# Kernel optimization log

Measured on AMD Instinct MI355X. Metric: run time of the kernel, lower is better.

The kernel has to match this reference:

```python
import jax, jax.numpy as jnp
import numpy as np

D_MODEL = 512; D_STATE = 128; D_CONV = 4; EXPAND = 2; HEADDIM = 64; CHUNK = 64
D_INNER = EXPAND * D_MODEL            # 1024
NHEADS = D_INNER // HEADDIM           # 16
CONV_DIM = D_INNER + 2 * D_STATE      # 1280
D_IN_PROJ = 2 * D_INNER + 2 * D_STATE + NHEADS  # 2320
BATCH, SEQLEN = 2, 8192


def setup_inputs() -> dict:
    key = jax.random.key(0)
    ks = jax.random.split(key, 8)
    s = 0.02
    return {
        "x": jax.random.normal(ks[0], (BATCH, SEQLEN, D_MODEL), jnp.float32),
        "in_proj_w": jax.random.normal(ks[1], (D_IN_PROJ, D_MODEL), jnp.float32) * s,
        "conv_w": jax.random.normal(ks[2], (CONV_DIM, 1, D_CONV), jnp.float32) * s,
        "conv_b": jnp.zeros((CONV_DIM,), jnp.float32),
        "dt_bias": jax.random.normal(ks[3], (NHEADS,), jnp.float32) * s,
        "A_log": jnp.log(jnp.arange(1, NHEADS + 1, dtype=jnp.float32)),
        "D_skip": jnp.ones((NHEADS,), jnp.float32),
        "norm_w": jnp.ones((D_INNER,), jnp.float32),
        "ssm_out_w": jax.random.normal(ks[4], (D_MODEL, D_INNER), jnp.float32) * s,
        "fuse_w": jax.random.normal(ks[5], (D_MODEL, 2 * D_MODEL), jnp.float32) * s,
        "fuse_b": jnp.zeros((D_MODEL,), jnp.float32),
    }


def segsum(a):
    # a: (..., T) -> (..., T, T) with [i, j] = sum_{j < d <= i} a[d]; -inf above diag
    T = a.shape[-1]
    a = jnp.broadcast_to(a[..., :, None], a.shape + (T,))
    a = jnp.where(jnp.tril(jnp.ones((T, T), bool), -1), a, 0.0)
    a = jnp.cumsum(a, axis=-2)
    return jnp.where(jnp.tril(jnp.ones((T, T), bool), 0), a, -jnp.inf)


def ssd(x, A, B, C):
    # x: (b,l,h,p), A: (b,l,h), B/C: (b,l,n) (single group, broadcast over heads)
    b, l, h, p = x.shape
    c = l // CHUNK
    x = x.reshape(b, c, CHUNK, h, p)
    A = jnp.transpose(A.reshape(b, c, CHUNK, h), (0, 3, 1, 2))   # (b,h,c,s)
    B = B.reshape(b, c, CHUNK, -1)
    C = C.reshape(b, c, CHUNK, -1)
    A_cumsum = jnp.cumsum(A, axis=-1)                             # (b,h,c,s)
    L = jnp.exp(segsum(A))                                        # (b,h,c,s,s) intra-chunk decay
    Y_diag = jnp.einsum("bcln,bcsn,bhcls,bcshp->bclhp", C, B, L, x)
    decay_states = jnp.exp(A_cumsum[..., -1:] - A_cumsum)         # (b,h,c,s)
    states = jnp.einsum("bcln,bhcl,bclhp->bchpn", B, decay_states, x)
    init = jnp.zeros_like(states[:, :1])
    A_pad = jnp.pad(A_cumsum[..., -1], ((0, 0), (0, 0), (1, 0)))  # (b,h,c+1)
    decay_chunk = jnp.exp(segsum(A_pad))                          # (b,h,c+1,c+1)
    new_states = jnp.einsum("bhzc,bchpn->bzhpn", decay_chunk,
                            jnp.concatenate([init, states], axis=1))
    states = new_states[:, :-1]                                   # state entering each chunk
    state_decay_out = jnp.exp(A_cumsum)
    Y_off = jnp.einsum("bchpn,bcsn,bhcs->bcshp", states, C, state_decay_out)
    return (Y_diag + Y_off).reshape(b, l, h, p)


def mamba2_block(u, in_proj_w, conv_w, conv_b, dt_bias, A_log, D_skip, norm_w, ssm_out_w):
    b, l, _ = u.shape
    zxbcdt = u @ in_proj_w.T                                      # (b,l,2320)
    z = zxbcdt[..., :D_INNER]
    xBC = zxbcdt[..., D_INNER:D_INNER + CONV_DIM]
    dt = jax.nn.softplus(zxbcdt[..., -NHEADS:] + dt_bias)         # (b,l,h)
    # depthwise causal conv over time
    conv = jax.lax.conv_general_dilated(
        jnp.transpose(xBC, (0, 2, 1)), conv_w, (1,), [(D_CONV - 1, 0)],
        dimension_numbers=("NCH", "OIH", "NCH"), feature_group_count=CONV_DIM)
    xBC = jax.nn.silu(jnp.transpose(conv + conv_b[None, :, None], (0, 2, 1)))
    xh = xBC[..., :D_INNER].reshape(b, l, NHEADS, HEADDIM)
    Bm = xBC[..., D_INNER:D_INNER + D_STATE]
    Cm = xBC[..., -D_STATE:]
    A = -jnp.exp(A_log)                                           # (h,)
    y = ssd(xh * dt[..., None], A * dt, Bm, Cm)
    y = y + xh * D_skip[None, None, :, None]
    y = y.reshape(b, l, D_INNER)
    # gated RMSNorm
    y = y * jax.nn.silu(z)
    y = y * jax.lax.rsqrt(jnp.mean(y * y, axis=-1, keepdims=True) + 1e-5) * norm_w
    return y @ ssm_out_w.T


def reference(x, in_proj_w, conv_w, conv_b, dt_bias, A_log, D_skip, norm_w,
              ssm_out_w, fuse_w, fuse_b):
    args = (in_proj_w, conv_w, conv_b, dt_bias, A_log, D_skip, norm_w, ssm_out_w)
    y_fwd = mamba2_block(x, *args)
    y_rev = jnp.flip(mamba2_block(jnp.flip(x, 1), *args), 1)
    y_cat = jnp.concatenate([y_fwd, y_rev], axis=-1)
    return y_cat @ fuse_w.T + fuse_b
```

## Files before the change

kernel.cpp:

```cpp
#include <hip/hip_runtime.h>
#include <cstddef>

#define B_SZ     2
#define L_SEQ    8192
#define D_INNERC 1024
#define D_CAT    2048
#define NHEADSC  16
#define CHUNKC   64
#define NCHUNKC  128
#define CONV_DIMC 1280
#define D_PROJC  2320
#define M_ROWS   16384

typedef unsigned short bfu;

using bf16x8 = __attribute__((ext_vector_type(8))) short;
using f32x4  = __attribute__((ext_vector_type(4))) float;

__device__ __forceinline__ float silu_(float v) { return v / (1.f + expf(-v)); }

__device__ __forceinline__ float b2f(bfu u) {
  return __uint_as_float((unsigned)u << 16);
}
__device__ __forceinline__ bfu f2b(float f) {
  unsigned x = __float_as_uint(f);
  return (bfu)((x + 0x7fffu + ((x >> 16) & 1u)) >> 16);
}

__device__ __forceinline__ float4 ld4(const float* p) { return *(const float4*)p; }
__device__ __forceinline__ float4 ld4(const bfu* p) {
  ushort4 u = *(const ushort4*)p;
  float4 f;
  f.x = b2f(u.x); f.y = b2f(u.y); f.z = b2f(u.z); f.w = b2f(u.w);
  return f;
}
__device__ __forceinline__ void st4(float* p, float4 v) { *(float4*)p = v; }
__device__ __forceinline__ void st4(bfu* p, float4 v) {
  ushort4 u;
  u.x = f2b(v.x); u.y = f2b(v.y); u.z = f2b(v.z); u.w = f2b(v.w);
  *(ushort4*)p = u;
}

__device__ __forceinline__ void gl_lds16(const bfu* g, bfu* l) {
  __builtin_amdgcn_global_load_lds(
      (const __attribute__((address_space(1))) unsigned int*)g,
      (__attribute__((address_space(3))) unsigned int*)l, 16, 0, 0);
}

__device__ __forceinline__ int pos_of(int b, int c, int l, int dir) {
  int t = c * CHUNKC + l;
  return dir ? (b * L_SEQ + (L_SEQ - 1) - t) : (b * L_SEQ + t);
}

__global__ __launch_bounds__(256)
void mfma_nt(const bfu* __restrict__ A, int lda,
             const bfu* __restrict__ Bw, int ldb,
             void* __restrict__ Cv, int ldc,
             int N, int K, const float* __restrict__ bias, int mode)
{
  __shared__ bfu sh[16384];
  bfu* As = sh;
  bfu* Bs = sh + 8192;
  const int tid  = threadIdx.x;
  const int lane = tid & 63;
  const int wave = __builtin_amdgcn_readfirstlane(tid >> 6);
  const int wm = wave & 1, wn = wave >> 1;

  const int num_n = gridDim.x;
  const int flat  = blockIdx.y * num_n + blockIdx.x;
  const int xcd   = flat & 7;
  const int g     = flat >> 3;
  const int n0 = (g % num_n) * 128;
  const int m0 = ((g / num_n) * 8 + xcd) * 128;

  f32x4 acc[4][4];
#pragma unroll
  for (int i = 0; i < 4; ++i)
#pragma unroll
    for (int j = 0; j < 4; ++j)
      acc[i][j] = (f32x4){0.f, 0.f, 0.f, 0.f};

  const int ro   = lane >> 3;
  const int slot = lane & 7;

  for (int k0 = 0; k0 < K; k0 += 64) {
    __syncthreads();
#pragma unroll
    for (int si = 0; si < 4; ++si) {
      int r = wave * 32 + si * 8 + ro;
      int cg = slot ^ (r & 7);
      gl_lds16(A  + (size_t)(m0 + r) * lda + k0 + cg * 8, As + (wave * 32 + si * 8) * 64);
      gl_lds16(Bw + (size_t)(n0 + r) * ldb + k0 + cg * 8, Bs + (wave * 32 + si * 8) * 64);
    }
    __syncthreads();

#pragma unroll
    for (int ks = 0; ks < 2; ++ks) {
      bf16x8 af[4], bfr[4];
#pragma unroll
      for (int i = 0; i < 4; ++i) {
        int ra = wm * 64 + i * 16 + (lane & 15);
        int ca = (ks * 4 + (lane >> 4)) ^ (ra & 7);
        af[i] = *(const bf16x8*)(As + ra * 64 + ca * 8);
        int rb = wn * 64 + i * 16 + (lane & 15);
        int cb = (ks * 4 + (lane >> 4)) ^ (rb & 7);
        bfr[i] = *(const bf16x8*)(Bs + rb * 64 + cb * 8);
      }
#pragma unroll
      for (int i = 0; i < 4; ++i)
#pragma unroll
        for (int j = 0; j < 4; ++j)
          acc[i][j] = __builtin_amdgcn_mfma_f32_16x16x32_bf16(af[i], bfr[j], acc[i][j], 0, 0, 0);
    }
  }

  __syncthreads();
  if (mode == 0) {
#pragma unroll
    for (int i = 0; i < 4; ++i)
#pragma unroll
      for (int j = 0; j < 4; ++j)
#pragma unroll
        for (int r = 0; r < 4; ++r) {
          int ml = wm * 64 + i * 16 + (lane >> 4) * 4 + r;
          int nl = wn * 64 + j * 16 + (lane & 15);
          sh[ml * 128 + nl] = f2b(acc[i][j][r]);
        }
    __syncthreads();
    bfu* Cb = (bfu*)Cv;
#pragma unroll
    for (int rr = 0; rr < 8; ++rr) {
      int idx = rr * 256 + tid;
      int row = idx >> 4, co = (idx & 15) * 8;
      if (n0 + co < N) {
        *(ulonglong2*)(Cb + (size_t)(m0 + row) * ldc + n0 + co) =
            *(const ulonglong2*)(sh + row * 128 + co);
      }
    }
  } else {
    float* Cf = (float*)Cv;
    float* shf = (float*)sh;
#pragma unroll
    for (int p = 0; p < 2; ++p) {
      if (wm == p) {
#pragma unroll
        for (int i = 0; i < 4; ++i)
#pragma unroll
          for (int j = 0; j < 4; ++j)
#pragma unroll
            for (int r = 0; r < 4; ++r) {
              int ml = i * 16 + (lane >> 4) * 4 + r;
              int nl = wn * 64 + j * 16 + (lane & 15);
              shf[ml * 128 + nl] = acc[i][j][r];
            }
      }
      __syncthreads();
#pragma unroll
      for (int rr = 0; rr < 8; ++rr) {
        int idx = rr * 256 + tid;
        int row = idx >> 5, co = (idx & 31) * 4;
        int n = n0 + co;
        if (n < N) {
          float4 v = *(float4*)(shf + row * 128 + co);
          float* cp = Cf + (size_t)(m0 + p * 64 + row) * ldc + n;
          if (bias) {
            v.x += bias[n]; v.y += bias[n + 1]; v.z += bias[n + 2]; v.w += bias[n + 3];
          }
          *(float4*)cp = v;
        }
      }
      __syncthreads();
    }
  }
}

__global__ __launch_bounds__(512)
void mfma_nt_8p(const bfu* __restrict__ A, int lda,
                const bfu* __restrict__ Bw, int ldb,
                bfu* __restrict__ C, int ldc, int N, int K)
{
  __shared__ bfu sh[65536];
  bfu* As0 = sh;
  bfu* As1 = sh + 16384;
  bfu* Bs0 = sh + 32768;
  bfu* Bs1 = sh + 49152;

  const int tid  = threadIdx.x;
  const int lane = tid & 63;
  const int w    = __builtin_amdgcn_readfirstlane(tid >> 6);
  const int wm = w & 1, wn = w >> 1;
  const int q = lane >> 4, t = lane & 15;

  const int num_n = gridDim.x;
  const int flat  = blockIdx.y * num_n + blockIdx.x;
  const int xcd   = flat & 7;
  const int g     = flat >> 3;
  const int n0 = (g % num_n) * 256;
  const int m0 = ((g / num_n) * 8 + xcd) * 256;

  auto STG = [&](const bfu* __restrict__ X, int ldx, int x0, int kt, int h,
                 bfu* dst) {
#pragma unroll
    for (int ci = 0; ci < 2; ++ci) {
      int rb = h * 128 + ci * 64 + w * 8;
      int r  = rb + (lane >> 3);
      int cg = (lane & 7) ^ (r & 7);
      gl_lds16(X + (size_t)(x0 + r) * ldx + kt * 64 + cg * 8, dst + rb * 64);
    }
  };
  auto FR = [&](const bfu* tile, int R, int gg) -> bf16x8 {
    return *(const bf16x8*)(tile + R * 64 + ((gg ^ (R & 7)) * 8));
  };

  f32x4 acc[8][4];
#pragma unroll
  for (int i = 0; i < 8; ++i)
#pragma unroll
    for (int j = 0; j < 4; ++j)
      acc[i][j] = (f32x4){0.f, 0.f, 0.f, 0.f};

  STG(Bw, ldb, n0, 0, 0, Bs0); STG(Bw, ldb, n0, 0, 1, Bs0);
  STG(A,  lda, m0, 0, 0, As0); STG(A,  lda, m0, 0, 1, As0);
  STG(Bw, ldb, n0, 1, 0, Bs1); STG(Bw, ldb, n0, 1, 1, Bs1);
  asm volatile("s_waitcnt vmcnt(4)" ::: "memory");
  __builtin_amdgcn_s_barrier();

  const int nIter = K >> 7;
  bf16x8 bfr[4][2];
  for (int it = 0; it < nIter; ++it) {
    const int kt = it * 2;
    const bool last = (it == nIter - 1);

#pragma unroll
    for (int p = 0; p < 4; ++p) {
      bf16x8 af[2][2];
#pragma unroll
      for (int ii = 0; ii < 2; ++ii)
#pragma unroll
        for (int ks = 0; ks < 2; ++ks)
          af[ii][ks] = FR(As0, wm * 128 + (2 * p + ii) * 16 + t, ks * 4 + q);
      if (p == 0) {
#pragma unroll
        for (int j = 0; j < 4; ++j)
#pragma unroll
          for (int ks = 0; ks < 2; ++ks)
            bfr[j][ks] = FR(Bs0, wn * 64 + j * 16 + t, ks * 4 + q);
      }
      if (p == 0)          STG(A,  lda, m0, kt + 1, 0, As1);
      if (p == 1)          STG(A,  lda, m0, kt + 1, 1, As1);
      if (p == 2 && !last) STG(Bw, ldb, n0, kt + 2, 0, Bs0);
      if (p == 3 && !last) STG(Bw, ldb, n0, kt + 2, 1, Bs0);
      if (p == 3) {
        if (last) asm volatile("s_waitcnt vmcnt(0)" ::: "memory");
        else      asm volatile("s_waitcnt vmcnt(4)" ::: "memory");
      }
      __builtin_amdgcn_s_barrier();
      __builtin_amdgcn_s_setprio(1);
#pragma unroll
      for (int ks = 0; ks < 2; ++ks)
#pragma unroll
        for (int ii = 0; ii < 2; ++ii)
#pragma unroll
          for (int j = 0; j < 4; ++j)
            acc[2 * p + ii][j] = __builtin_amdgcn_mfma_f32_16x16x32_bf16(
                af[ii][ks], bfr[j][ks], acc[2 * p + ii][j], 0, 0, 0);
      __builtin_amdgcn_s_setprio(0);
      __builtin_amdgcn_s_barrier();
    }

#pragma unroll
    for (int p = 0; p < 4; ++p) {
      bf16x8 af[2][2];
#pragma unroll
      for (int ii = 0; ii < 2; ++ii)
#pragma unroll
        for (int ks = 0; ks < 2; ++ks)
          af[ii][ks] = FR(As1, wm * 128 + (2 * p + ii) * 16 + t, ks * 4 + q);
      if (p == 0) {
#pragma unroll
        for (int j = 0; j < 4; ++j)
#pragma unroll
          for (int ks = 0; ks < 2; ++ks)
            bfr[j][ks] = FR(Bs1, wn * 64 + j * 16 + t, ks * 4 + q);
      }
      if (p == 0 && !last) STG(A,  lda, m0, kt + 2, 0, As0);
      if (p == 1 && !last) STG(A,  lda, m0, kt + 2, 1, As0);
      if (p == 2 && !last) STG(Bw, ldb, n0, kt + 3, 0, Bs1);
      if (p == 3 && !last) STG(Bw, ldb, n0, kt + 3, 1, Bs1);
      if (p == 3 && !last) asm volatile("s_waitcnt vmcnt(4)" ::: "memory");
      __builtin_amdgcn_s_barrier();
      __builtin_amdgcn_s_setprio(1);
#pragma unroll
      for (int ks = 0; ks < 2; ++ks)
#pragma unroll
        for (int ii = 0; ii < 2; ++ii)
#pragma unroll
          for (int j = 0; j < 4; ++j)
            acc[2 * p + ii][j] = __builtin_amdgcn_mfma_f32_16x16x32_bf16(
                af[ii][ks], bfr[j][ks], acc[2 * p + ii][j], 0, 0, 0);
      __builtin_amdgcn_s_setprio(0);
      __builtin_amdgcn_s_barrier();
    }
  }

#pragma unroll
  for (int i = 0; i < 8; ++i)
#pragma unroll
    for (int j = 0; j < 4; ++j)
#pragma unroll
      for (int r = 0; r < 4; ++r) {
        int ml = wm * 128 + i * 16 + q * 4 + r;
        int nl = wn * 64 + j * 16 + t;
        sh[ml * 256 + nl] = f2b(acc[i][j][r]);
      }
  __syncthreads();
#pragma unroll
  for (int rr = 0; rr < 16; ++rr) {
    int idx = rr * 512 + tid;
    int row = idx >> 5, co = (idx & 31) * 8;
    if (n0 + co < N) {
      *(ulonglong2*)(C + (size_t)(m0 + row) * ldc + n0 + co) =
          *(const ulonglong2*)(sh + row * 256 + co);
    }
  }
}

__global__ __launch_bounds__(256)
void cvt_x_k(const float* __restrict__ in, bfu* __restrict__ out)
{
  int q = blockIdx.x * 256 + threadIdx.x;
  st4(out + (size_t)q * 4, ld4(in + (size_t)q * 4));
}

__global__ __launch_bounds__(256)
void cvt_w_k(const float* __restrict__ in, bfu* __restrict__ out)
{
  int q = blockIdx.x * 256 + threadIdx.x;
  int row = q >> 7, c4 = (q & 127) << 2;
  float4 v = {0.f, 0.f, 0.f, 0.f};
  if (row < D_PROJC) v = ld4(in + (size_t)row * 512 + c4);
  st4(out + (size_t)row * 512 + c4, v);
}

__global__ __launch_bounds__(256)
void transpose_k(const float* __restrict__ in, bfu* __restrict__ out)
{
  int idx = blockIdx.x * 256 + threadIdx.x;
  int j = idx >> 9, k = idx & 511;
  out[idx] = f2b(in[k * 1024 + j]);
}

__global__ __launch_bounds__(256)
void cvt_fuse_k(const float* __restrict__ in, bfu* __restrict__ out)
{
  int q = blockIdx.x * 256 + threadIdx.x;
  int m = q >> 7, kg = (q & 127) << 2;
  int o = m >> 1, dir = m & 1;
  float4 v = ld4(in + (size_t)o * 1024 + dir * 512 + kg);
  st4(out + (size_t)m * 512 + kg, v);
}

__global__ __launch_bounds__(256)
void conv_k(const bfu* __restrict__ zx, const float* __restrict__ conv_w,
            const float* __restrict__ conv_b, bfu* __restrict__ xBC,
            size_t xbc_str, int dir_lo)
{
  int di  = blockIdx.y >> 11;
  int dir = dir_lo + di;
  bfu* xBCd = xBC + (size_t)di * xbc_str;
  int ch = blockIdx.x * 256 + threadIdx.x;
  int m0 = (blockIdx.y & 2047) * 8;
  int b  = m0 >> 13, tb = m0 & (L_SEQ - 1);
  float w0 = conv_w[ch * 4 + 0], w1 = conv_w[ch * 4 + 1];
  float w2 = conv_w[ch * 4 + 2], w3 = conv_w[ch * 4 + 3];
  float cb = conv_b[ch];
  const bfu* src = zx + 1024 + ch;
  const int shift = dir ? 0 : 3;

  float v[11];
#pragma unroll
  for (int i = 0; i < 11; ++i) {
    int tt = tb + i - shift;
    v[i] = (tt >= 0 && tt < L_SEQ)
         ? b2f(src[(size_t)(b * L_SEQ + tt) * D_PROJC]) : 0.f;
  }
#pragma unroll
  for (int j = 0; j < 8; ++j) {
    float acc = cb;
    if (dir == 0) {
      acc += w0 * v[j] + w1 * v[j + 1] + w2 * v[j + 2] + w3 * v[j + 3];
    } else {
      acc += w0 * v[j + 3] + w1 * v[j + 2] + w2 * v[j + 1] + w3 * v[j];
    }
    xBCd[(size_t)(m0 + j) * CONV_DIMC + ch] = f2b(silu_(acc));
  }
}

__global__ __launch_bounds__(256)
void states_mfma_k(const bfu* __restrict__ zx, const bfu* __restrict__ xBC,
                   size_t xbc_str,
                   const float* __restrict__ dt_bias, const float* __restrict__ A_log,
                   float* __restrict__ acum_g, float* __restrict__ dt_g,
                   size_t ac_str,
                   bfu* __restrict__ states, size_t st_str, int dir_lo)
{
  __shared__ bfu BT[128 * 72];
  __shared__ bfu xsT[64 * 72];
  __shared__ float scaleS[8 * 64];

  int di  = blockIdx.x >> 9;
  int dir = dir_lo + di;
  const bfu* xBCd = xBC + (size_t)di * xbc_str;
  float* acumd = acum_g + (size_t)di * ac_str;
  float* dtgd  = dt_g   + (size_t)di * ac_str;
  bfu* statesd = states + (size_t)di * st_str;

  int bid = blockIdx.x & 511;
  int hb = bid >> 8;
  int c = bid & 127, b = (bid >> 7) & 1;
  int tid = threadIdx.x, lane = tid & 63;
  int w = tid >> 6, q = lane >> 4, t = lane & 15;

#pragma unroll
  for (int rr = 0; rr < 2; ++rr) {
    int i = w + rr * 4;
    int h = hb * 8 + i;
    int l = lane;
    int pos = pos_of(b, c, l, dir);
    float dtr = b2f(zx[(size_t)pos * D_PROJC + 2304 + h]) + dt_bias[h];
    float dt = (dtr > 20.f) ? dtr : log1pf(expf(dtr));
    float a = -expf(A_log[h]) * dt;
#pragma unroll
    for (int off = 1; off < 64; off <<= 1) {
      float v = __shfl_up(a, off);
      if (l >= off) a += v;
    }
    float alast = __shfl(a, 63);
    int gi = ((b * NCHUNKC + c) * NHEADSC + h) * 64 + l;
    acumd[gi] = a; dtgd[gi] = dt;
    scaleS[i * 64 + l] = dt * expf(alast - a);
  }

#pragma unroll
  for (int r = 0; r < 8; ++r) {
    int qq = tid + r * 256;
    int l = qq & 63, ng = qq >> 6;
    ushort4 v = *(const ushort4*)(xBCd + (size_t)pos_of(b, c, l, dir) * CONV_DIMC + 1024 + ng * 4);
    BT[(ng * 4 + 0) * 72 + l] = v.x; BT[(ng * 4 + 1) * 72 + l] = v.y;
    BT[(ng * 4 + 2) * 72 + l] = v.z; BT[(ng * 4 + 3) * 72 + l] = v.w;
  }

  ushort4 xr[4];
  auto PREFX = [&](int i) {
    int h = hb * 8 + i;
#pragma unroll
    for (int r = 0; r < 4; ++r) {
      int qq = tid + r * 256;
      int l = qq & 63, pg = qq >> 6;
      xr[r] = *(const ushort4*)(xBCd + (size_t)pos_of(b, c, l, dir) * CONV_DIMC + h * 64 + pg * 4);
    }
  };
  PREFX(0);
  __syncthreads();

  for (int i = 0; i < 8; ++i) {
    int h = hb * 8 + i;
#pragma unroll
    for (int r = 0; r < 4; ++r) {
      int qq = tid + r * 256;
      int l = qq & 63, pg = qq >> 6;
      float s = scaleS[i * 64 + l];
      ushort4 v = xr[r];
      xsT[(pg * 4 + 0) * 72 + l] = f2b(b2f(v.x) * s);
      xsT[(pg * 4 + 1) * 72 + l] = f2b(b2f(v.y) * s);
      xsT[(pg * 4 + 2) * 72 + l] = f2b(b2f(v.z) * s);
      xsT[(pg * 4 + 3) * 72 + l] = f2b(b2f(v.w) * s);
    }
    if (i < 7) PREFX(i + 1);
    __syncthreads();

    bf16x8 axs[2];
#pragma unroll
    for (int ks = 0; ks < 2; ++ks)
      axs[ks] = *(const bf16x8*)(xsT + (w * 16 + t) * 72 + ks * 32 + q * 8);

    f32x4 acc[8];
#pragma unroll
    for (int j = 0; j < 8; ++j) acc[j] = (f32x4){0.f, 0.f, 0.f, 0.f};
#pragma unroll
    for (int ks = 0; ks < 2; ++ks)
#pragma unroll
      for (int j = 0; j < 8; ++j) {
        bf16x8 bB = *(const bf16x8*)(BT + (j * 16 + t) * 72 + ks * 32 + q * 8);
        acc[j] = __builtin_amdgcn_mfma_f32_16x16x32_bf16(axs[ks], bB, acc[j], 0, 0, 0);
      }

    size_t base = ((size_t)(b * NCHUNKC + c) * NHEADSC + h) * 8192;
#pragma unroll
    for (int j = 0; j < 8; ++j)
#pragma unroll
      for (int r = 0; r < 4; ++r) {
        int p = w * 16 + q * 4 + r, n = j * 16 + t;
        statesd[base + p * 128 + n] = f2b(acc[j][r]);
      }
    __syncthreads();
  }
}

__global__ __launch_bounds__(256)
void scan_k(bfu* __restrict__ states, size_t st_str,
            const float* __restrict__ acum_g, size_t ac_str)
{
  int di  = blockIdx.x >> 9;
  int bid = blockIdx.x & 511;
  bfu* statesd = states + (size_t)di * st_str;
  const float* acumd = acum_g + (size_t)di * ac_str;

  int eb = bid & 15, h = (bid >> 4) & 15, b = bid >> 8;
  int e = eb * 512 + threadIdx.x * 2;
  bfu* p0 = statesd + ((size_t)(b * NCHUNKC) * NHEADSC + h) * 8192 + e;
  const float* ac = acumd + ((b * NCHUNKC) * NHEADSC + h) * 64 + 63;
  const size_t cstride = (size_t)NHEADSC * 8192;
  const int astride = NHEADSC * 64;

  float pre0 = 0.f, pre1 = 0.f;
  uint raw = *(const uint*)p0;
  float dcur = expf(ac[0]);
  for (int c = 0; c < NCHUNKC; ++c) {
    uint raw_next = 0; float dnext = 0.f;
    if (c < NCHUNKC - 1) {
      raw_next = *(const uint*)(p0 + (c + 1) * cstride);
      dnext = expf(ac[(c + 1) * astride]);
    }
    float v0 = b2f((bfu)(raw & 0xffff));
    float v1 = b2f((bfu)(raw >> 16));
    uint packed = (uint)f2b(pre0) | ((uint)f2b(pre1) << 16);
    *(uint*)(p0 + c * cstride) = packed;
    pre0 = v0 + dcur * pre0;
    pre1 = v1 + dcur * pre1;
    raw = raw_next; dcur = dnext;
  }
}

__global__ __launch_bounds__(256)
void y_mfma_k(const bfu* __restrict__ xBC, size_t xbc_str,
              const bfu* __restrict__ states, size_t st_str,
              const float* __restrict__ acum_g, const float* __restrict__ dt_g,
              size_t ac_str,
              const float* __restrict__ D_skip, bfu* __restrict__ ycat, int dir_lo)
{
  __shared__ bfu smem[30976];
  bfu* Cs  = smem;
  bfu* Bsc = smem + 8704;
  bfu* Ps  = smem + 17408;
  bfu* xhT = smem + 26112;
  float* acumH = (float*)(smem + 30720);
  float* dtH   = acumH + 64;

  int di  = blockIdx.x >> 9;
  int dir = dir_lo + di;
  const bfu* xBCd = xBC + (size_t)di * xbc_str;
  const bfu* statesd = states + (size_t)di * st_str;
  const float* acumd = acum_g + (size_t)di * ac_str;
  const float* dtgd  = dt_g   + (size_t)di * ac_str;

  int bid = blockIdx.x & 511;
  int hb = bid >> 8;
  int c = bid & 127, b = (bid >> 7) & 1;
  int tid = threadIdx.x, lane = tid & 63;
  int w = tid >> 6, q = lane >> 4, t = lane & 15;

#pragma unroll
  for (int r = 0; r < 8; ++r) {
    int qq = tid + r * 256;
    int row = qq >> 5, grp = qq & 31;
    const bfu* src = xBCd + (size_t)pos_of(b, c, row, dir) * CONV_DIMC;
    *(ushort4*)(Cs  + row * 136 + grp * 4) = *(const ushort4*)(src + 1152 + grp * 4);
    *(ushort4*)(Bsc + row * 136 + grp * 4) = *(const ushort4*)(src + 1024 + grp * 4);
  }
  __syncthreads();

  bf16x8 af[4];
#pragma unroll
  for (int ks = 0; ks < 4; ++ks)
    af[ks] = *(const bf16x8*)(Cs + (w * 16 + t) * 136 + ks * 32 + q * 8);

  f32x4 sacc[4];
#pragma unroll
  for (int j = 0; j < 4; ++j) sacc[j] = (f32x4){0.f, 0.f, 0.f, 0.f};
#pragma unroll
  for (int ks = 0; ks < 4; ++ks)
#pragma unroll
    for (int j = 0; j < 4; ++j) {
      bf16x8 bf = *(const bf16x8*)(Bsc + (j * 16 + t) * 136 + ks * 32 + q * 8);
      sacc[j] = __builtin_amdgcn_mfma_f32_16x16x32_bf16(af[ks], bf, sacc[j], 0, 0, 0);
    }

  for (int i = 0; i < 8; ++i) {
    int h = hb * 8 + i;
    __syncthreads();
    size_t pbase = ((size_t)(b * NCHUNKC + c) * NHEADSC + h) * 8192;
#pragma unroll
    for (int r = 0; r < 8; ++r) {
      int qq = tid + r * 256;
      int row = qq >> 5, grp = qq & 31;
      *(ushort4*)(Ps + row * 136 + grp * 4) =
          *(const ushort4*)(statesd + pbase + row * 128 + grp * 4);
    }
#pragma unroll
    for (int r = 0; r < 4; ++r) {
      int qq = tid + r * 256;
      int l = qq & 63, pg = qq >> 6;
      ushort4 v = *(const ushort4*)(xBCd + (size_t)pos_of(b, c, l, dir) * CONV_DIMC + h * 64 + pg * 4);
      xhT[(pg * 4 + 0) * 72 + l] = v.x; xhT[(pg * 4 + 1) * 72 + l] = v.y;
      xhT[(pg * 4 + 2) * 72 + l] = v.z; xhT[(pg * 4 + 3) * 72 + l] = v.w;
    }
    if (tid < 64) {
      int gi = ((b * NCHUNKC + c) * NHEADSC + h) * 64 + tid;
      acumH[tid] = acumd[gi]; dtH[tid] = dtgd[gi];
    }
    __syncthreads();

    f32x4 yacc[4];
#pragma unroll
    for (int j = 0; j < 4; ++j) yacc[j] = (f32x4){0.f, 0.f, 0.f, 0.f};
#pragma unroll
    for (int ks = 0; ks < 4; ++ks)
#pragma unroll
      for (int j = 0; j < 4; ++j) {
        bf16x8 bP = *(const bf16x8*)(Ps + (j * 16 + t) * 136 + ks * 32 + q * 8);
        yacc[j] = __builtin_amdgcn_mfma_f32_16x16x32_bf16(af[ks], bP, yacc[j], 0, 0, 0);
      }

    float Dh = D_skip[h];
    bfu* sc = Bsc;
#pragma unroll
    for (int j = 0; j < 4; ++j)
#pragma unroll
      for (int r = 0; r < 4; ++r) {
        int l = w * 16 + q * 4 + r, s = j * 16 + t;
        float v = 0.f;
        if (s <= l) v = sacc[j][r] * expf(acumH[l] - acumH[s]) * dtH[s];
        if (s == l) v += Dh;
        sc[l * 72 + s] = f2b(v);
      }

    f32x4 acc2[4];
    float dec[4];
#pragma unroll
    for (int r = 0; r < 4; ++r) dec[r] = expf(acumH[w * 16 + q * 4 + r]);
#pragma unroll
    for (int j = 0; j < 4; ++j)
#pragma unroll
      for (int r = 0; r < 4; ++r) acc2[j][r] = yacc[j][r] * dec[r];

#pragma unroll
    for (int ks = 0; ks < 2; ++ks) {
      bf16x8 asc = *(const bf16x8*)(sc + (w * 16 + t) * 72 + ks * 32 + q * 8);
#pragma unroll
      for (int j = 0; j < 4; ++j) {
        bf16x8 bx = *(const bf16x8*)(xhT + (j * 16 + t) * 72 + ks * 32 + q * 8);
        acc2[j] = __builtin_amdgcn_mfma_f32_16x16x32_bf16(asc, bx, acc2[j], 0, 0, 0);
      }
    }

#pragma unroll
    for (int j = 0; j < 4; ++j)
#pragma unroll
      for (int r = 0; r < 4; ++r) {
        int l = w * 16 + q * 4 + r, p = j * 16 + t;
        ycat[(size_t)pos_of(b, c, l, dir) * D_CAT + dir * 1024 + h * 64 + p] =
            f2b(acc2[j][r]);
      }
  }
}

__global__ __launch_bounds__(256)
void norm_k(bfu* __restrict__ ycat, const bfu* __restrict__ zx,
            const float* __restrict__ norm_w, int dir_lo)
{
  int di  = blockIdx.x >> 14;
  int dir = dir_lo + di;
  int m = blockIdx.x & 16383, tid = threadIdx.x;
  bfu* yp = ycat + (size_t)m * D_CAT + dir * 1024 + tid * 4;
  float4 y = ld4(yp);
  float4 z = ld4(zx + (size_t)m * D_PROJC + tid * 4);
  float4 g;
  g.x = y.x * silu_(z.x); g.y = y.y * silu_(z.y);
  g.z = y.z * silu_(z.z); g.w = y.w * silu_(z.w);
  float ss = g.x * g.x + g.y * g.y + g.z * g.z + g.w * g.w;
#pragma unroll
  for (int off = 32; off >= 1; off >>= 1) ss += __shfl_xor(ss, off);
  __shared__ float red[4];
  int wid = tid >> 6;
  if ((tid & 63) == 0) red[wid] = ss;
  __syncthreads();
  float tot = red[0] + red[1] + red[2] + red[3];
  float scale = rsqrtf(tot * (1.f / 1024.f) + 1e-5f);
  float4 w = *(const float4*)(norm_w + tid * 4);
  g.x *= scale * w.x; g.y *= scale * w.y; g.z *= scale * w.z; g.w *= scale * w.w;
  st4(yp, g);
}

extern "C" void kernel_launch(void* const* d_in, const int* in_sizes, int n_in,
                              void* d_out, int out_size, void* d_ws, size_t ws_size,
                              hipStream_t stream)
{
  const float* x         = (const float*)d_in[0];
  const float* in_proj_w = (const float*)d_in[1];
  const float* conv_w    = (const float*)d_in[2];
  const float* conv_b    = (const float*)d_in[3];
  const float* dt_bias   = (const float*)d_in[4];
  const float* A_log     = (const float*)d_in[5];
  const float* D_skip    = (const float*)d_in[6];
  const float* norm_w    = (const float*)d_in[7];
  const float* ssm_out_w = (const float*)d_in[8];
  const float* fuse_w    = (const float*)d_in[9];
  const float* fuse_b    = (const float*)d_in[10];
  float* out = (float*)d_out;

  const size_t ZX_E  = (size_t)M_ROWS * D_PROJC;
  const size_t XBC_E = (size_t)M_ROWS * CONV_DIMC;
  const size_t ST_E  = 33554432;
  const size_t YC_E  = (size_t)M_ROWS * D_CAT;
  const size_t AC_E  = 262144;

  size_t need2 = (ZX_E + 2 * XBC_E + 2 * ST_E + YC_E + 2 * 524288 + 1048576) * 2
               + 4 * AC_E * 4;
  const int nd = (ws_size >= need2) ? 2 : 1;

  bfu* zx     = (bfu*)d_ws;
  bfu* xBC    = zx + ZX_E;
  bfu* states = xBC + (size_t)nd * XBC_E;
  bfu* ycat   = states + (size_t)nd * ST_E;
  float* acum = (float*)(ycat + YC_E);
  float* dtg  = acum + (size_t)nd * AC_E;
  bfu* ssmTb  = (bfu*)(dtg + (size_t)nd * AC_E);
  bfu* fuseA  = ssmTb + 524288;
  bfu* wcmb   = fuseA + 524288;
  bfu* xb = states;
  bfu* wb = states + 8388608;

  const size_t xbc_str = (nd == 2) ? XBC_E : 0;
  const size_t st_str  = (nd == 2) ? ST_E  : 0;
  const size_t ac_str  = (nd == 2) ? AC_E  : 0;

  cvt_x_k<<<8192, 256, 0, stream>>>(x, xb);
  cvt_w_k<<<1280, 256, 0, stream>>>(in_proj_w, wb);
  transpose_k<<<2048, 256, 0, stream>>>(ssm_out_w, ssmTb);
  cvt_fuse_k<<<512, 256, 0, stream>>>(fuse_w, fuseA);

  mfma_nt<<<dim3(8, 8), 256, 0, stream>>>(
      fuseA, 512, ssmTb, 512, wcmb, 1024, 1024, 512, nullptr, 0);

  mfma_nt_8p<<<dim3(10, 64), 512, 0, stream>>>(
      xb, 512, wb, 512, zx, D_PROJC, D_PROJC, 512);

  for (int dl = 0; dl < 2; dl += nd) {
    conv_k<<<dim3(5, 2048 * nd), 256, 0, stream>>>(
        zx, conv_w, conv_b, xBC, xbc_str, dl);
    states_mfma_k<<<512 * nd, 256, 0, stream>>>(
        zx, xBC, xbc_str, dt_bias, A_log, acum, dtg, ac_str, states, st_str, dl);
    scan_k<<<512 * nd, 256, 0, stream>>>(states, st_str, acum, ac_str);
    y_mfma_k<<<512 * nd, 256, 0, stream>>>(
        xBC, xbc_str, states, st_str, acum, dtg, ac_str, D_skip, ycat, dl);
    norm_k<<<16384 * nd, 256, 0, stream>>>(ycat, zx, norm_w, dl);
  }

  mfma_nt<<<dim3(4, 128), 256, 0, stream>>>(
      ycat, D_CAT, wcmb, D_CAT, out, 512, 512, D_CAT, fuse_b, 1);
}
```

Baseline: 521.1 us.

## Fuse gated RMSNorm into y_mfma kernel by processing all heads per block

The y computation kernel now loops over all 16 heads for one (batch, chunk), applies the silu(z) gate inline, and accumulates per-row sums of squares. It then rescales its own rows in place with the RMS scale and norm weights, and the separate norm kernel launch is removed. This avoids a separate pass and launch over ycat and zx, but halves the grid size and serializes twice as many heads per block, reducing parallelism.

Result: slower. 600.0 us (+15.1%).

```diff
diff --git a/kernel.cpp b/kernel.cpp
--- a/kernel.cpp
+++ b/kernel.cpp
@@ -546,27 +546,29 @@
 void y_mfma_k(const bfu* __restrict__ xBC, size_t xbc_str,
               const bfu* __restrict__ states, size_t st_str,
               const float* __restrict__ acum_g, const float* __restrict__ dt_g,
-              size_t ac_str,
-              const float* __restrict__ D_skip, bfu* __restrict__ ycat, int dir_lo)
-{
-  __shared__ bfu smem[30976];
+              size_t ac_str, const float* __restrict__ D_skip,
+              const bfu* __restrict__ zx, const float* __restrict__ norm_w,
+              bfu* __restrict__ ycat, int dir_lo)
+{
+  __shared__ bfu smem[35712];
   bfu* Cs  = smem;
   bfu* Bsc = smem + 8704;
   bfu* Ps  = smem + 17408;
   bfu* xhT = smem + 26112;
-  float* acumH = (float*)(smem + 30720);
-  float* dtH   = acumH + 64;
-
-  int di  = blockIdx.x >> 9;
+  bfu* zs  = smem + 30720;
+  float* acumH  = (float*)(smem + 35328);
+  float* dtH    = acumH + 64;
+  float* scaleL = dtH + 64;
+
+  int di  = blockIdx.x >> 8;
   int dir = dir_lo + di;
   const bfu* xBCd = xBC + (size_t)di * xbc_str;
   const bfu* statesd = states + (size_t)di * st_str;
   const float* acumd = acum_g + (size_t)di * ac_str;
   const float* dtgd  = dt_g   + (size_t)di * ac_str;
 
-  int bid = blockIdx.x & 511;
-  int hb = bid >> 8;
-  int c = bid & 127, b = (bid >> 7) & 1;
+  int bid = blockIdx.x & 255;
+  int c = bid & 127, b = bid >> 7;
   int tid = threadIdx.x, lane = tid & 63;
   int w = tid >> 6, q = lane >> 4, t = lane & 15;
 
@@ -596,8 +598,9 @@
       sacc[j] = __builtin_amdgcn_mfma_f32_16x16x32_bf16(af[ks], bf, sacc[j], 0, 0, 0);
     }
 
-  for (int i = 0; i < 8; ++i) {
-    int h = hb * 8 + i;
+  float ssp[4] = {0.f, 0.f, 0.f, 0.f};
+
+  for (int h = 0; h < NHEADSC; ++h) {
     __syncthreads();
     size_t pbase = ((size_t)(b * NCHUNKC + c) * NHEADSC + h) * 8192;
 #pragma unroll
@@ -615,6 +618,13 @@
       xhT[(pg * 4 + 0) * 72 + l] = v.x; xhT[(pg * 4 + 1) * 72 + l] = v.y;
       xhT[(pg * 4 + 2) * 72 + l] = v.z; xhT[(pg * 4 + 3) * 72 + l] = v.w;
     }
+#pragma unroll
+    for (int r = 0; r < 4; ++r) {
+      int qq = tid + r * 256;
+      int row = qq >> 4, cg = qq & 15;
+      *(ushort4*)(zs + row * 72 + cg * 4) =
+          *(const ushort4*)(zx + (size_t)pos_of(b, c, row, dir) * D_PROJC + h * 64 + cg * 4);
+    }
     if (tid < 64) {
       int gi = ((b * NCHUNKC + c) * NHEADSC + h) * 64 + tid;
       acumH[tid] = acumd[gi]; dtH[tid] = dtgd[gi];
@@ -669,37 +679,46 @@
 #pragma unroll
       for (int r = 0; r < 4; ++r) {
         int l = w * 16 + q * 4 + r, p = j * 16 + t;
+        float g = acc2[j][r] * silu_(b2f(zs[l * 72 + p]));
+        ssp[r] += g * g;
         ycat[(size_t)pos_of(b, c, l, dir) * D_CAT + dir * 1024 + h * 64 + p] =
-            f2b(acc2[j][r]);
-      }
-  }
-}
-
-__global__ __launch_bounds__(256)
-void norm_k(bfu* __restrict__ ycat, const bfu* __restrict__ zx,
-            const float* __restrict__ norm_w, int dir_lo)
-{
-  int di  = blockIdx.x >> 14;
-  int dir = dir_lo + di;
-  int m = blockIdx.x & 16383, tid = threadIdx.x;
-  bfu* yp = ycat + (size_t)m * D_CAT + dir * 1024 + tid * 4;
-  float4 y = ld4(yp);
-  float4 z = ld4(zx + (size_t)m * D_PROJC + tid * 4);
-  float4 g;
-  g.x = y.x * silu_(z.x); g.y = y.y * silu_(z.y);
-  g.z = y.z * silu_(z.z); g.w = y.w * silu_(z.w);
-  float ss = g.x * g.x + g.y * g.y + g.z * g.z + g.w * g.w;
-#pragma unroll
-  for (int off = 32; off >= 1; off >>= 1) ss += __shfl_xor(ss, off);
-  __shared__ float red[4];
-  int wid = tid >> 6;
-  if ((tid & 63) == 0) red[wid] = ss;
+            f2b(g);
+      }
+  }
+
+#pragma unroll
+  for (int r = 0; r < 4; ++r) {
+#pragma unroll
+    for (int off = 1; off < 16; off <<= 1) ssp[r] += __shfl_xor(ssp[r], off);
+  }
+  if (t == 0) {
+#pragma unroll
+    for (int r = 0; r < 4; ++r) {
+      int l = w * 16 + q * 4 + r;
+      scaleL[l] = rsqrtf(ssp[r] * (1.f / 1024.f) + 1e-5f);
+    }
+  }
+  __threadfence_block();
   __syncthreads();
-  float tot = red[0] + red[1] + red[2] + red[3];
-  float scale = rsqrtf(tot * (1.f / 1024.f) + 1e-5f);
-  float4 w = *(const float4*)(norm_w + tid * 4);
-  g.x *= scale * w.x; g.y *= scale * w.y; g.z *= scale * w.z; g.w *= scale * w.w;
-  st4(yp, g);
+
+#pragma unroll
+  for (int it = 0; it < 32; ++it) {
+    int idx = it * 256 + tid;
+    int row = idx >> 7, co = (idx & 127) * 8;
+    bfu* yp = ycat + (size_t)pos_of(b, c, row, dir) * D_CAT + dir * 1024 + co;
+    ushort4 v0 = *(const ushort4*)yp;
+    ushort4 v1 = *(const ushort4*)(yp + 4);
+    float s = scaleL[row];
+    float4 w0 = *(const float4*)(norm_w + co);
+    float4 w1 = *(const float4*)(norm_w + co + 4);
+    ushort4 o0, o1;
+    o0.x = f2b(b2f(v0.x) * s * w0.x); o0.y = f2b(b2f(v0.y) * s * w0.y);
+    o0.z = f2b(b2f(v0.z) * s * w0.z); o0.w = f2b(b2f(v0.w) * s * w0.w);
+    o1.x = f2b(b2f(v1.x) * s * w1.x); o1.y = f2b(b2f(v1.y) * s * w1.y);
+    o1.z = f2b(b2f(v1.z) * s * w1.z); o1.w = f2b(b2f(v1.w) * s * w1.w);
+    *(ushort4*)yp = o0;
+    *(ushort4*)(yp + 4) = o1;
+  }
 }
 
 extern "C" void kernel_launch(void* const* d_in, const int* in_sizes, int n_in,
@@ -762,9 +781,9 @@
     states_mfma_k<<<512 * nd, 256, 0, stream>>>(
         zx, xBC, xbc_str, dt_bias, A_log, acum, dtg, ac_str, states, st_str, dl);
     scan_k<<<512 * nd, 256, 0, stream>>>(states, st_str, acum, ac_str);
-    y_mfma_k<<<512 * nd, 256, 0, stream>>>(
-        xBC, xbc_str, states, st_str, acum, dtg, ac_str, D_skip, ycat, dl);
-    norm_k<<<16384 * nd, 256, 0, stream>>>(ycat, zx, norm_w, dl);
+    y_mfma_k<<<256 * nd, 256, 0, stream>>>(
+        xBC, xbc_str, states, st_str, acum, dtg, ac_str, D_skip,
+        zx, norm_w, ycat, dl);
   }
 
   mfma_nt<<<dim3(4, 128), 256, 0, stream>>>(
```
